# Kernel tuning notes

Hardware: AMD Instinct MI355X
Metric: run time of the kernel (lower is better)

## Reference

```python
import jax, jax.numpy as jnp
import numpy as np
from jax import lax

# Mamba2-130m-like config (quantized wrapper)
D_MODEL = 768
N_LAYER = 8
D_STATE = 128
D_CONV = 4
EXPAND = 2
HEADDIM = 64
VOCAB = 50288
D_INNER = EXPAND * D_MODEL            # 1536
NHEADS = D_INNER // HEADDIM           # 24
D_IN_PROJ = 2 * D_INNER + 2 * D_STATE + NHEADS  # 3352 (ngroups=1)
CONV_DIM = D_INNER + 2 * D_STATE      # 1792
EPS = 1e-5
BATCH, SEQLEN = 1, 1024

# QuantRMSNorm rsqrt lookup table (256 entries over [1e-5, 10])
LUT_X = jnp.linspace(1e-5, 10.0, 256)
LUT_Y = 1.0 / jnp.sqrt(LUT_X)


def _fake_quant_linear(w):
    # QuantLinear: torch.quantize_per_tensor(scale=0.1, zero_point=0, qint8).dequantize()
    return jnp.clip(jnp.round(w / 0.1), -128, 127) * 0.1


def setup_inputs():
    key = jax.random.key(0)
    ks = jax.random.split(key, 12)
    input_ids = jax.random.randint(ks[0], (BATCH, SEQLEN), 0, VOCAB)
    embedding = jax.random.normal(ks[1], (VOCAB, D_MODEL), jnp.float32)
    norm_w = jnp.ones((N_LAYER, D_MODEL), jnp.float32)
    in_proj_w = _fake_quant_linear(
        jax.random.normal(ks[2], (N_LAYER, D_IN_PROJ, D_MODEL), jnp.float32) * (D_MODEL ** -0.5))
    # QuantConv1d: asymmetric per-tensor int8 weight; forward uses q_weight.float()
    # WITHOUT subtracting zero_point (as in the source), times (w_scale * x_scale).
    conv_f = jax.random.normal(ks[3], (N_LAYER, CONV_DIM, D_CONV), jnp.float32) * (D_CONV ** -0.5)
    wmin = conv_f.min(axis=(1, 2), keepdims=True)
    wmax = conv_f.max(axis=(1, 2), keepdims=True)
    conv_scale = (wmax - wmin) / (255.0 + 1e-8)   # qmax - qmin = 255
    zp = jnp.round(-wmin / conv_scale)
    q_conv_w = jnp.clip(jnp.round(conv_f / conv_scale) + zp, -128, 127)
    conv_scale = conv_scale.reshape(N_LAYER)
    conv_b = jax.random.normal(ks[4], (N_LAYER, CONV_DIM), jnp.float32) * 0.02
    dt = jax.random.uniform(ks[5], (N_LAYER, NHEADS), jnp.float32, 0.001, 0.1)
    dt_bias = jnp.log(jnp.expm1(dt))              # inverse softplus
    A_log = jnp.log(jax.random.uniform(ks[6], (N_LAYER, NHEADS), jnp.float32, 1.0, 16.0))
    D_param = jnp.ones((N_LAYER, NHEADS), jnp.float32)
    mixer_norm_w = jnp.ones((N_LAYER, D_INNER), jnp.float32)
    out_proj_w = _fake_quant_linear(
        jax.random.normal(ks[7], (N_LAYER, D_MODEL, D_INNER), jnp.float32) * (D_INNER ** -0.5))
    normf_w = jnp.ones((D_MODEL,), jnp.float32)
    lm_head_w = _fake_quant_linear(
        jax.random.normal(ks[8], (VOCAB, D_MODEL), jnp.float32) * (D_MODEL ** -0.5))
    return dict(input_ids=input_ids, embedding=embedding, norm_w=norm_w, in_proj_w=in_proj_w,
                q_conv_w=q_conv_w, conv_scale=conv_scale, conv_b=conv_b, dt_bias=dt_bias,
                A_log=A_log, D_param=D_param, mixer_norm_w=mixer_norm_w, out_proj_w=out_proj_w,
                normf_w=normf_w, lm_head_w=lm_head_w)


def _lut_rmsnorm(x, w):
    # QuantRMSNorm: rsqrt approximated by a 256-entry LUT via bucketize
    rms = jnp.mean(x * x, axis=-1, keepdims=True) + EPS       # [b,l,1]
    idx = jnp.clip(jnp.searchsorted(LUT_X, rms), 0, 255)      # torch.bucketize (right=False)
    return x * LUT_Y[idx] * w


def _quant_act(x):
    # quantize_activation: symmetric per-tensor int8
    s = jnp.max(jnp.abs(x)) / (127.0 + 1e-8)
    return jnp.clip(jnp.round(x / s), -128, 127), s


def _mixer(u, in_w, qcw, cscale, cb, dtb, a_log, d_p, mnw, out_w):
    b, l, _ = u.shape
    zxbcdt = jnp.einsum('bld,ed->ble', u, in_w)               # QuantLinear (pre-fake-quantized w)
    z = zxbcdt[..., :D_INNER]
    xBC = zxbcdt[..., D_INNER:D_INNER + CONV_DIM]
    dt = jax.nn.softplus(zxbcdt[..., -NHEADS:] + dtb)         # [b,l,h]
    # QuantConv1d: depthwise causal conv on int8-quantized activation
    xq, xs = _quant_act(xBC)
    xp = jnp.pad(xq, ((0, 0), (D_CONV - 1, 0), (0, 0)))
    conv = sum(xp[:, k:k + l, :] * qcw[:, k] for k in range(D_CONV)) + cb
    xBC = jax.nn.silu(conv * (cscale * xs))
    x = xBC[..., :D_INNER].reshape(b, l, NHEADS, HEADDIM)
    Bm = xBC[..., D_INNER:D_INNER + D_STATE]                  # ngroups=1, shared over heads
    Cm = xBC[..., D_INNER + D_STATE:]
    dA = dt * (-jnp.exp(a_log))                               # [b,l,h]
    xdt = x * dt[..., None]
    def step(hs, inp):
        xdt_t, dA_t, B_t, C_t = inp
        hs = jnp.exp(dA_t)[..., None, None] * hs + xdt_t[..., None] * B_t[:, None, None, :]
        return hs, jnp.einsum('bhpn,bn->bhp', hs, C_t)
    h0 = jnp.zeros((b, NHEADS, HEADDIM, D_STATE), u.dtype)
    _, ys = lax.scan(step, h0, (xdt.swapaxes(0, 1), dA.swapaxes(0, 1),
                                Bm.swapaxes(0, 1), Cm.swapaxes(0, 1)))
    y = ys.swapaxes(0, 1) + x * d_p[None, None, :, None]      # [b,l,h,p]
    y = y.reshape(b, l, D_INNER)
    y = y * jax.nn.silu(z)                                    # gated RMSNorm (float, not LUT)
    y = y * lax.rsqrt(jnp.mean(y * y, axis=-1, keepdims=True) + EPS) * mnw
    return jnp.einsum('ble,de->bld', y, out_w)                # QuantLinear out_proj


def reference(input_ids, embedding, norm_w, in_proj_w, q_conv_w, conv_scale, conv_b,
              dt_bias, A_log, D_param, mixer_norm_w, out_proj_w, normf_w, lm_head_w):
    x = embedding[input_ids]
    for i in range(N_LAYER):
        y = _mixer(_lut_rmsnorm(x, norm_w[i]), in_proj_w[i], q_conv_w[i], conv_scale[i],
                   conv_b[i], dt_bias[i], A_log[i], D_param[i], mixer_norm_w[i], out_proj_w[i])
        x = y + x
    x = _lut_rmsnorm(x, normf_w)
    return jnp.einsum('bld,vd->blv', x, lm_head_w)            # logits [b,l,vocab]
```

## Files before the change

### kernel.cpp

```cpp
#include <hip/hip_runtime.h>
#include <math.h>

#define D_MODEL 768
#define N_LAYER 8
#define D_STATE 128
#define D_CONV 4
#define HEADDIM 64
#define D_INNER 1536
#define NHEADS 24
#define D_IN_PROJ 3352
#define CONV_DIM 1792
#define SEQLEN 1024
#define VOCAB 50288
#define EPS 1e-5f
#define T_SEG 32
#define NSEG  32
#define INP_PAD 3456
#define VOC_PAD 50304

typedef __bf16 bf16x8 __attribute__((ext_vector_type(8)));
typedef float f32x4 __attribute__((ext_vector_type(4)));

__device__ inline unsigned short f2bf(float x) {
    union { float f; unsigned u; } v; v.f = x;
    unsigned r = v.u + 0x7fffu + ((v.u >> 16) & 1u);
    return (unsigned short)(r >> 16);
}
__device__ inline float bf2f(unsigned short b) {
    union { unsigned u; float f; } v; v.u = ((unsigned)b) << 16;
    return v.f;
}

__device__ __forceinline__ void gld16(unsigned short* lds, const unsigned short* g) {
    __builtin_amdgcn_global_load_lds(
        (const __attribute__((address_space(1))) unsigned int*)g,
        (__attribute__((address_space(3))) unsigned int*)lds, 16, 0, 0);
}

__global__ void k_embed(const int* __restrict__ ids, const float* __restrict__ emb,
                        float* __restrict__ x) {
    int t = blockIdx.x;
    int id = ids[t];
    const float* er = emb + (long)id * D_MODEL;
    for (int d = threadIdx.x; d < D_MODEL; d += blockDim.x)
        x[(long)t * D_MODEL + d] = er[d];
}

__global__ void k_wq(const float* __restrict__ src, unsigned short* __restrict__ dst,
                     int n8_per_layer, int nlayer, long dst_stride8) {
    long total = (long)n8_per_layer * nlayer;
    for (long i = (long)blockIdx.x * 256 + threadIdx.x; i < total; i += (long)gridDim.x * 256) {
        long lay = i / n8_per_layer;
        long e = i - lay * n8_per_layer;
        const float* s = src + (lay * n8_per_layer + e) * 8;
        float4 a = *(const float4*)s, b = *(const float4*)(s + 4);
        float ff[8] = {a.x, a.y, a.z, a.w, b.x, b.y, b.z, b.w};
        unsigned short h[8];
#pragma unroll
        for (int j = 0; j < 8; ++j) h[j] = f2bf(rintf(ff[j] * 10.0f));
        *(uint4*)(dst + (lay * dst_stride8 + e) * 8) =
            make_uint4(h[0] | (h[1] << 16), h[2] | (h[3] << 16),
                       h[4] | (h[5] << 16), h[6] | (h[7] << 16));
    }
}

__global__ void k_lutnorm(const float* __restrict__ x, const float* __restrict__ w,
                          unsigned short* __restrict__ oh, unsigned short* __restrict__ ol,
                          unsigned* __restrict__ mx) {
    __shared__ float sbuf[256];
    int t = blockIdx.x;
    if (t == 0 && threadIdx.x == 0) *mx = 0u;
    const float* xr = x + (long)t * D_MODEL;
    float ss = 0.f;
    for (int d = threadIdx.x; d < D_MODEL; d += 256) { float v = xr[d]; ss += v * v; }
    sbuf[threadIdx.x] = ss; __syncthreads();
    for (int s = 128; s > 0; s >>= 1) {
        if (threadIdx.x < s) sbuf[threadIdx.x] += sbuf[threadIdx.x + s];
        __syncthreads();
    }
    float rms = sbuf[0] / (float)D_MODEL + EPS;
    const float X0 = 1e-5f;
    const float STEP = (10.0f - 1e-5f) / 255.0f;
    int idx = (int)ceilf((rms - X0) / STEP);
    idx = min(max(idx, 0), 255);
    while (idx > 0 && (X0 + (float)(idx - 1) * STEP) >= rms) --idx;
    while (idx < 255 && (X0 + (float)idx * STEP) < rms) ++idx;
    float scale = 1.0f / sqrtf(X0 + (float)idx * STEP);
    for (int d = threadIdx.x; d < D_MODEL; d += 256) {
        float v = xr[d] * scale * w[d];
        unsigned short h = f2bf(v);
        oh[(long)t * D_MODEL + d] = h;
        ol[(long)t * D_MODEL + d] = f2bf(v - bf2f(h));
    }
}

template <int BM, int BN, int PASSES, bool AMAX, bool ACCUM, int MT>
__global__ __launch_bounds__(256) void k_gemm(
    const unsigned short* __restrict__ Ah_g, const unsigned short* __restrict__ Al_g,
    const unsigned short* __restrict__ Bq_g, float* __restrict__ C,
    int N, int NT, int K, unsigned* __restrict__ mx) {

    const int i = blockIdx.x;
    const int rxcd = i & 7;
    const int xm = (i >> 3) % MT;
    const int q = i / (8 * MT);
    const int y = q * 8 + rxcd;
    if (y >= NT) return;
    const int bm = xm * BM, bn = y * BN;

    constexpr int MR = BM / 32;
    constexpr int NR = BN / 32;
    constexpr int ASL = 4 * BM;
    constexpr int BSL = 4 * BN;

    __shared__ __align__(16) unsigned short AhL[ASL * 8];
    __shared__ __align__(16) unsigned short AlL[(PASSES == 2) ? ASL * 8 : 8];
    __shared__ __align__(16) unsigned short BqL[BSL * 8];

    const int tid = threadIdx.x;
    const int w = tid >> 6, l = tid & 63;
    const int wm = w >> 1, wn = w & 1;
    const int lr = l & 15, lg = l >> 4;

    f32x4 acc[MR][NR];
#pragma unroll
    for (int m = 0; m < MR; ++m)
#pragma unroll
        for (int n = 0; n < NR; ++n) acc[m][n] = (f32x4){0.f, 0.f, 0.f, 0.f};

    for (int k0 = 0; k0 < K; k0 += 32) {
#pragma unroll
        for (int j = 0; j < ASL / 256; ++j) {
            int s = j * 256 + tid;
            int g = s / BM, r = s - g * BM;
            size_t goff = (size_t)(bm + r) * K + k0 + g * 8;
            gld16(&AhL[s * 8], Ah_g + goff);
            if constexpr (PASSES == 2) gld16(&AlL[s * 8], Al_g + goff);
        }
#pragma unroll
        for (int j = 0; j < BSL / 256; ++j) {
            int s = j * 256 + tid;
            int g = s / BN, r = s - g * BN;
            gld16(&BqL[s * 8], Bq_g + (size_t)(bn + r) * K + k0 + g * 8);
        }
        __syncthreads();

        bf16x8 ah[MR], al[MR], bh[NR];
#pragma unroll
        for (int m = 0; m < MR; ++m) {
            int row = wm * (BM / 2) + m * 16 + lr;
            ah[m] = *(const bf16x8*)&AhL[(lg * BM + row) * 8];
            if constexpr (PASSES == 2) al[m] = *(const bf16x8*)&AlL[(lg * BM + row) * 8];
        }
#pragma unroll
        for (int n = 0; n < NR; ++n) {
            int row = wn * (BN / 2) + n * 16 + lr;
            bh[n] = *(const bf16x8*)&BqL[(lg * BN + row) * 8];
        }
#pragma unroll
        for (int m = 0; m < MR; ++m)
#pragma unroll
            for (int n = 0; n < NR; ++n) {
                acc[m][n] = __builtin_amdgcn_mfma_f32_16x16x32_bf16(ah[m], bh[n], acc[m][n], 0, 0, 0);
                if constexpr (PASSES == 2)
                    acc[m][n] = __builtin_amdgcn_mfma_f32_16x16x32_bf16(al[m], bh[n], acc[m][n], 0, 0, 0);
            }
        __syncthreads();
    }

    float lmax = 0.f;
#pragma unroll
    for (int m = 0; m < MR; ++m) {
        int row0 = bm + wm * (BM / 2) + m * 16 + lg * 4;
#pragma unroll
        for (int n = 0; n < NR; ++n) {
            int col = bn + wn * (BN / 2) + n * 16 + lr;
            if (col < N) {
#pragma unroll
                for (int r4 = 0; r4 < 4; ++r4) {
                    float v = acc[m][n][r4] * 0.1f;
                    if (AMAX && col >= D_INNER) lmax = fmaxf(lmax, fabsf(v));
                    size_t off = (size_t)(row0 + r4) * N + col;
                    if (ACCUM) C[off] += v; else C[off] = v;
                }
            }
        }
    }
    if (AMAX) {
#pragma unroll
        for (int sh = 1; sh <= 32; sh <<= 1) lmax = fmaxf(lmax, __shfl_xor(lmax, sh));
        if (l == 0) atomicMax(mx, __float_as_uint(lmax));
    }
}

__global__ void k_convq(const float* __restrict__ zx, const float* __restrict__ qcw,
                        const float* __restrict__ cb, const float* __restrict__ cscale,
                        const unsigned* __restrict__ mx, float* __restrict__ xact) {
    int i = blockIdx.x * blockDim.x + threadIdx.x;
    if (i >= SEQLEN * CONV_DIM) return;
    float s = __uint_as_float(*mx) / (127.0f + 1e-8f);
    float inv_s = 1.0f / s;
    int t = i / CONV_DIM, c = i - t * CONV_DIM;
    float acc = cb[c];
#pragma unroll
    for (int k = 0; k < D_CONV; ++k) {
        int tt = t - (D_CONV - 1) + k;
        if (tt >= 0) {
            float q = rintf(zx[(size_t)tt * D_IN_PROJ + D_INNER + c] * inv_s);
            q = fminf(fmaxf(q, -128.0f), 127.0f);
            acc = fmaf(q, qcw[c * D_CONV + k], acc);
        }
    }
    float v = acc * (cscale[0] * s);
    xact[i] = v / (1.0f + expf(-v));
}

__global__ __launch_bounds__(256) void k_scan_local(
    const float* __restrict__ xact, const float* __restrict__ zx,
    const float* __restrict__ dtbias, const float* __restrict__ A_log,
    float* __restrict__ y, float* __restrict__ hloc, float* __restrict__ dpre) {
    const int head = blockIdx.x;
    const int seg  = blockIdx.y;
    const int tid  = threadIdx.x;
    const int p  = tid >> 2;
    const int nc = tid & 3;
    const int t0 = seg * T_SEG;

    __shared__ float4 sB4[T_SEG][32];
    __shared__ float4 sC4[T_SEG][32];
    __shared__ float  sX[T_SEG][64];
    __shared__ float  sDt[T_SEG], sA[T_SEG];

#pragma unroll
    for (int it = 0; it < 4; ++it) {
        int slot = tid + it * 256;
        int t = slot >> 5, c4 = slot & 31;
        const float* rowp = xact + (size_t)(t0 + t) * CONV_DIM + D_INNER;
        float4 bv = *(const float4*)(rowp + c4 * 4);
        float4 cv = *(const float4*)(rowp + D_STATE + c4 * 4);
        int grp = c4 >> 3, r4 = c4 & 7;
        int sl = grp * 8 + ((r4 + 2 * grp) & 7);
        sB4[t][sl] = bv;
        sC4[t][sl] = cv;
    }
#pragma unroll
    for (int it = 0; it < 2; ++it) {
        int slot = tid + it * 256;
        int t = slot >> 4, c4 = slot & 15;
        *(float4*)&sX[t][c4 * 4] =
            *(const float4*)(xact + (size_t)(t0 + t) * CONV_DIM + head * HEADDIM + c4 * 4);
    }
    if (tid < T_SEG) {
        float v = zx[(size_t)(t0 + tid) * D_IN_PROJ + (D_INNER + CONV_DIM) + head] + dtbias[head];
        float dtv = fmaxf(v, 0.f) + log1pf(expf(-fabsf(v)));
        sDt[tid] = dtv;
        sA[tid] = expf(dtv * (-expf(A_log[head])));
    }
    __syncthreads();

    float h[32];
#pragma unroll
    for (int j = 0; j < 32; ++j) h[j] = 0.f;
    float d = 1.f;
    float* yrow = y + head * HEADDIM + p;

    for (int t = 0; t < T_SEG; ++t) {
        float a = sA[t], dtv = sDt[t];
        float xdt = sX[t][p] * dtv;
        d *= a;
        float acc = 0.f;
#pragma unroll
        for (int j4 = 0; j4 < 8; ++j4) {
            int sl = nc * 8 + ((j4 + 2 * nc) & 7);
            float4 Bv = sB4[t][sl];
            float4 Cv = sC4[t][sl];
            h[j4 * 4 + 0] = fmaf(a, h[j4 * 4 + 0], xdt * Bv.x); acc = fmaf(h[j4 * 4 + 0], Cv.x, acc);
            h[j4 * 4 + 1] = fmaf(a, h[j4 * 4 + 1], xdt * Bv.y); acc = fmaf(h[j4 * 4 + 1], Cv.y, acc);
            h[j4 * 4 + 2] = fmaf(a, h[j4 * 4 + 2], xdt * Bv.z); acc = fmaf(h[j4 * 4 + 2], Cv.z, acc);
            h[j4 * 4 + 3] = fmaf(a, h[j4 * 4 + 3], xdt * Bv.w); acc = fmaf(h[j4 * 4 + 3], Cv.w, acc);
        }
        acc += __shfl_xor(acc, 1);
        acc += __shfl_xor(acc, 2);
        if (nc == 0) yrow[(size_t)(t0 + t) * D_INNER] = acc;
        if (tid == 0) dpre[(head * NSEG + seg) * T_SEG + t] = d;
    }

    float* hb = hloc + ((size_t)(head * NSEG + seg) * 64 + p) * 128 + nc * 32;
#pragma unroll
    for (int j4 = 0; j4 < 8; ++j4)
        *(float4*)(hb + j4 * 4) =
            make_float4(h[j4 * 4], h[j4 * 4 + 1], h[j4 * 4 + 2], h[j4 * 4 + 3]);
}

__global__ __launch_bounds__(256) void k_scan_seg(float* __restrict__ hloc,
                                                  const float* __restrict__ dpre) {
    int g = blockIdx.x * 256 + threadIdx.x;
    int head = g >> 11;
    int e4 = g & 2047;
    float4 run = make_float4(0.f, 0.f, 0.f, 0.f);
    for (int seg = 0; seg < NSEG; ++seg) {
        float d = dpre[(head * NSEG + seg) * T_SEG + (T_SEG - 1)];
        float4* ptr = (float4*)hloc + (size_t)(head * NSEG + seg) * 2048 + e4;
        float4 v = *ptr;
        run.x = fmaf(d, run.x, v.x);
        run.y = fmaf(d, run.y, v.y);
        run.z = fmaf(d, run.z, v.z);
        run.w = fmaf(d, run.w, v.w);
        *ptr = run;
    }
}

__global__ __launch_bounds__(256) void k_scan_fix(
    const float* __restrict__ xact, const float* __restrict__ hloc,
    const float* __restrict__ dpre, float* __restrict__ y) {
    const int head = blockIdx.x;
    const int seg  = blockIdx.y + 1;
    const int tid  = threadIdx.x;
    const int p  = tid >> 2;
    const int nc = tid & 3;
    const int t0 = seg * T_SEG;

    __shared__ float4 sC4[T_SEG][32];
    __shared__ float  sD[T_SEG];

#pragma unroll
    for (int it = 0; it < 4; ++it) {
        int slot = tid + it * 256;
        int t = slot >> 5, c4 = slot & 31;
        float4 cv = *(const float4*)(xact + (size_t)(t0 + t) * CONV_DIM + D_INNER + D_STATE + c4 * 4);
        int grp = c4 >> 3, r4 = c4 & 7;
        sC4[t][grp * 8 + ((r4 + 2 * grp) & 7)] = cv;
    }
    if (tid < T_SEG) sD[tid] = dpre[(head * NSEG + seg) * T_SEG + tid];
    __syncthreads();

    float H[32];
    const float* hb = hloc + ((size_t)(head * NSEG + seg - 1) * 64 + p) * 128 + nc * 32;
#pragma unroll
    for (int j4 = 0; j4 < 8; ++j4) {
        float4 v = *(const float4*)(hb + j4 * 4);
        H[j4 * 4 + 0] = v.x; H[j4 * 4 + 1] = v.y; H[j4 * 4 + 2] = v.z; H[j4 * 4 + 3] = v.w;
    }
    float* yrow = y + head * HEADDIM + p;
    for (int t = 0; t < T_SEG; ++t) {
        float acc = 0.f;
#pragma unroll
        for (int j4 = 0; j4 < 8; ++j4) {
            int sl = nc * 8 + ((j4 + 2 * nc) & 7);
            float4 Cv = sC4[t][sl];
            acc = fmaf(H[j4 * 4 + 0], Cv.x, acc);
            acc = fmaf(H[j4 * 4 + 1], Cv.y, acc);
            acc = fmaf(H[j4 * 4 + 2], Cv.z, acc);
            acc = fmaf(H[j4 * 4 + 3], Cv.w, acc);
        }
        acc += __shfl_xor(acc, 1);
        acc += __shfl_xor(acc, 2);
        if (nc == 0) yrow[(size_t)(t0 + t) * D_INNER] += sD[t] * acc;
    }
}

__global__ void k_gatenorm(const float* __restrict__ ybuf, const float* __restrict__ zx,
                           const float* __restrict__ xact, const float* __restrict__ dpar,
                           const float* __restrict__ mnw,
                           unsigned short* __restrict__ y3h, unsigned short* __restrict__ y3l) {
    __shared__ float sbuf[256];
    int t = blockIdx.x;
    const float* yr = ybuf + (long)t * D_INNER;
    const float* zr = zx + (long)t * D_IN_PROJ;
    const float* xa = xact + (long)t * CONV_DIM;
    float vals[6];
    float ss = 0.f;
#pragma unroll
    for (int j = 0; j < 6; ++j) {
        int e = threadIdx.x + j * 256;
        float z = zr[e];
        float v = (yr[e] + xa[e] * dpar[e >> 6]) * (z / (1.0f + expf(-z)));
        vals[j] = v; ss += v * v;
    }
    sbuf[threadIdx.x] = ss; __syncthreads();
    for (int s = 128; s > 0; s >>= 1) {
        if (threadIdx.x < s) sbuf[threadIdx.x] += sbuf[threadIdx.x + s];
        __syncthreads();
    }
    float scale = 1.0f / sqrtf(sbuf[0] / (float)D_INNER + EPS);
#pragma unroll
    for (int j = 0; j < 6; ++j) {
        int e = threadIdx.x + j * 256;
        float v = vals[j] * scale * mnw[e];
        unsigned short h = f2bf(v);
        y3h[(long)t * D_INNER + e] = h;
        y3l[(long)t * D_INNER + e] = f2bf(v - bf2f(h));
    }
}

extern "C" void kernel_launch(void* const* d_in, const int* in_sizes, int n_in,
                              void* d_out, int out_size, void* d_ws, size_t ws_size,
                              hipStream_t stream) {
    const int*   ids    = (const int*)d_in[0];
    const float* emb    = (const float*)d_in[1];
    const float* norm_w = (const float*)d_in[2];
    const float* inw    = (const float*)d_in[3];
    const float* qconv  = (const float*)d_in[4];
    const float* cscale = (const float*)d_in[5];
    const float* convb  = (const float*)d_in[6];
    const float* dtbias = (const float*)d_in[7];
    const float* alog   = (const float*)d_in[8];
    const float* dpar   = (const float*)d_in[9];
    const float* mnw    = (const float*)d_in[10];
    const float* outw   = (const float*)d_in[11];
    const float* normf  = (const float*)d_in[12];
    const float* lmw    = (const float*)d_in[13];
    float* out = (float*)d_out;

    char* base = (char*)d_ws;
    size_t off = 0;
    auto alloc = [&](size_t bytes) { char* r = base + off; off = (off + bytes + 255) & ~(size_t)255; return r; };

    float* xres = (float*)alloc((size_t)SEQLEN * D_MODEL * 4);
    float* zx   = (float*)alloc((size_t)SEQLEN * D_IN_PROJ * 4);
    float* xact = (float*)alloc((size_t)SEQLEN * CONV_DIM * 4);
    float* ybuf = (float*)alloc((size_t)SEQLEN * D_INNER * 4);
    float* hloc = (float*)alloc((size_t)NHEADS * NSEG * HEADDIM * D_STATE * 4);
    float* dpre = (float*)alloc((size_t)NHEADS * NSEG * T_SEG * 4);
    unsigned* mx = (unsigned*)alloc(64);
    unsigned short* uh  = (unsigned short*)alloc((size_t)SEQLEN * D_MODEL * 2);
    unsigned short* ul  = (unsigned short*)alloc((size_t)SEQLEN * D_MODEL * 2);
    unsigned short* y3h = (unsigned short*)alloc((size_t)SEQLEN * D_INNER * 2);
    unsigned short* y3l = (unsigned short*)alloc((size_t)SEQLEN * D_INNER * 2);
    unsigned short* inwq  = (unsigned short*)alloc((size_t)N_LAYER * INP_PAD * D_MODEL * 2);
    unsigned short* outwq = (unsigned short*)alloc((size_t)N_LAYER * D_MODEL * D_INNER * 2);
    unsigned short* lmwq  = (unsigned short*)alloc((size_t)VOC_PAD * D_MODEL * 2);

    k_embed<<<SEQLEN, 256, 0, stream>>>(ids, emb, xres);
    k_wq<<<2048, 256, 0, stream>>>(inw, inwq, D_IN_PROJ * D_MODEL / 8, N_LAYER,
                                   (long)INP_PAD * D_MODEL / 8);
    k_wq<<<2048, 256, 0, stream>>>(outw, outwq, D_MODEL * D_INNER / 8, N_LAYER,
                                   (long)D_MODEL * D_INNER / 8);
    k_wq<<<2048, 256, 0, stream>>>(lmw, lmwq, VOCAB * D_MODEL / 8, 1,
                                   (long)VOC_PAD * D_MODEL / 8);

    int nq = SEQLEN * CONV_DIM;
    for (int l = 0; l < N_LAYER; ++l) {
        k_lutnorm<<<SEQLEN, 256, 0, stream>>>(xres, norm_w + l * D_MODEL, uh, ul, mx);
        k_gemm<128, 128, 2, true, false, 8><<<256, 256, 0, stream>>>(
            uh, ul, inwq + (size_t)l * INP_PAD * D_MODEL, zx, D_IN_PROJ, 27, D_MODEL, mx);
        k_convq<<<(nq + 255) / 256, 256, 0, stream>>>(zx, qconv + l * CONV_DIM * D_CONV,
                                                      convb + l * CONV_DIM, cscale + l, mx, xact);
        dim3 gs1(NHEADS, NSEG);
        k_scan_local<<<gs1, 256, 0, stream>>>(xact, zx, dtbias + l * NHEADS, alog + l * NHEADS,
                                              ybuf, hloc, dpre);
        k_scan_seg<<<192, 256, 0, stream>>>(hloc, dpre);
        dim3 gs3(NHEADS, NSEG - 1);
        k_scan_fix<<<gs3, 256, 0, stream>>>(xact, hloc, dpre, ybuf);
        k_gatenorm<<<SEQLEN, 256, 0, stream>>>(ybuf, zx, xact, dpar + l * NHEADS,
                                               mnw + l * D_INNER, y3h, y3l);
        k_gemm<64, 64, 2, false, true, 16><<<256, 256, 0, stream>>>(
            y3h, y3l, outwq + (size_t)l * D_MODEL * D_INNER, xres, D_MODEL, 12, D_INNER, nullptr);
    }
    k_lutnorm<<<SEQLEN, 256, 0, stream>>>(xres, normf, uh, ul, mx);
    k_gemm<128, 128, 1, false, false, 8><<<3200, 256, 0, stream>>>(
        uh, nullptr, lmwq, out, VOCAB, 393, D_MODEL, nullptr);
}
```

Measured before the change: 1.738 ms.

## Replace LDS-staged GEMM with register-direct MFMA GEMM and split-K atomics

Rewrites the GEMM so each wave loads its A and B fragments straight from global memory into registers and prefetches the next k-step, dropping LDS staging and block-wide barriers. Out_proj switches to split-K with atomicAdd into the residual, and the in_proj and lm_head tiles are resized, with weight padding enlarged to match. Without LDS, operands are no longer shared across waves, so global and L2 traffic goes up. Atomics make the accumulation order nondeterministic. NK is hardcoded to 24, which only matches K/KSPLIT=768.

```diff
diff --git a/kernel.cpp b/kernel.cpp
--- a/kernel.cpp
+++ b/kernel.cpp
@@ -15,8 +15,8 @@
 #define EPS 1e-5f
 #define T_SEG 32
 #define NSEG  32
-#define INP_PAD 3456
-#define VOC_PAD 50304
+#define INP_PAD2 3584
+#define VOC_PAD2 50432
 
 typedef __bf16 bf16x8 __attribute__((ext_vector_type(8)));
 typedef float f32x4 __attribute__((ext_vector_type(4)));
@@ -30,11 +30,8 @@
     union { unsigned u; float f; } v; v.u = ((unsigned)b) << 16;
     return v.f;
 }
-
-__device__ __forceinline__ void gld16(unsigned short* lds, const unsigned short* g) {
-    __builtin_amdgcn_global_load_lds(
-        (const __attribute__((address_space(1))) unsigned int*)g,
-        (__attribute__((address_space(3))) unsigned int*)lds, 16, 0, 0);
+__device__ __forceinline__ bf16x8 asbf8(uint4 v) {
+    return __builtin_bit_cast(bf16x8, v);
 }
 
 __global__ void k_embed(const int* __restrict__ ids, const float* __restrict__ emb,
@@ -94,94 +91,106 @@
     }
 }
 
-template <int BM, int BN, int PASSES, bool AMAX, bool ACCUM, int MT>
-__global__ __launch_bounds__(256) void k_gemm(
+template <int WMR, int WNR, int PASSES, bool AMAX, int KSPLIT, bool ATOMIC, int MTILES>
+__global__ __launch_bounds__(256) void k_gemm_reg(
     const unsigned short* __restrict__ Ah_g, const unsigned short* __restrict__ Al_g,
     const unsigned short* __restrict__ Bq_g, float* __restrict__ C,
-    int N, int NT, int K, unsigned* __restrict__ mx) {
+    int N, int NCT, int K, unsigned* __restrict__ mx) {
 
     const int i = blockIdx.x;
     const int rxcd = i & 7;
-    const int xm = (i >> 3) % MT;
-    const int q = i / (8 * MT);
-    const int y = q * 8 + rxcd;
-    if (y >= NT) return;
-    const int bm = xm * BM, bn = y * BN;
-
-    constexpr int MR = BM / 32;
-    constexpr int NR = BN / 32;
-    constexpr int ASL = 4 * BM;
-    constexpr int BSL = 4 * BN;
-
-    __shared__ __align__(16) unsigned short AhL[ASL * 8];
-    __shared__ __align__(16) unsigned short AlL[(PASSES == 2) ? ASL * 8 : 8];
-    __shared__ __align__(16) unsigned short BqL[BSL * 8];
+    int rest = i >> 3;
+    const int xm = rest % MTILES; rest /= MTILES;
+    const int ks = rest % KSPLIT; rest /= KSPLIT;
+    const int y = rest * 8 + rxcd;
+    if (y >= NCT) return;
 
     const int tid = threadIdx.x;
     const int w = tid >> 6, l = tid & 63;
-    const int wm = w >> 1, wn = w & 1;
     const int lr = l & 15, lg = l >> 4;
 
-    f32x4 acc[MR][NR];
-#pragma unroll
-    for (int m = 0; m < MR; ++m)
-#pragma unroll
-        for (int n = 0; n < NR; ++n) acc[m][n] = (f32x4){0.f, 0.f, 0.f, 0.f};
-
-    for (int k0 = 0; k0 < K; k0 += 32) {
-#pragma unroll
-        for (int j = 0; j < ASL / 256; ++j) {
-            int s = j * 256 + tid;
-            int g = s / BM, r = s - g * BM;
-            size_t goff = (size_t)(bm + r) * K + k0 + g * 8;
-            gld16(&AhL[s * 8], Ah_g + goff);
-            if constexpr (PASSES == 2) gld16(&AlL[s * 8], Al_g + goff);
-        }
-#pragma unroll
-        for (int j = 0; j < BSL / 256; ++j) {
-            int s = j * 256 + tid;
-            int g = s / BN, r = s - g * BN;
-            gld16(&BqL[s * 8], Bq_g + (size_t)(bn + r) * K + k0 + g * 8);
-        }
-        __syncthreads();
-
-        bf16x8 ah[MR], al[MR], bh[NR];
-#pragma unroll
-        for (int m = 0; m < MR; ++m) {
-            int row = wm * (BM / 2) + m * 16 + lr;
-            ah[m] = *(const bf16x8*)&AhL[(lg * BM + row) * 8];
-            if constexpr (PASSES == 2) al[m] = *(const bf16x8*)&AlL[(lg * BM + row) * 8];
-        }
-#pragma unroll
-        for (int n = 0; n < NR; ++n) {
-            int row = wn * (BN / 2) + n * 16 + lr;
-            bh[n] = *(const bf16x8*)&BqL[(lg * BN + row) * 8];
-        }
-#pragma unroll
-        for (int m = 0; m < MR; ++m)
-#pragma unroll
-            for (int n = 0; n < NR; ++n) {
-                acc[m][n] = __builtin_amdgcn_mfma_f32_16x16x32_bf16(ah[m], bh[n], acc[m][n], 0, 0, 0);
+    const int bm = xm * (WMR * 16);
+    const int bn = y * (4 * WNR * 16) + w * (WNR * 16);
+    const int kbeg = ks * (K / KSPLIT);
+    constexpr int NK = 24;
+
+    const unsigned short* ah_p[WMR];
+    const unsigned short* al_p[WMR];
+    const unsigned short* b_p[WNR];
+#pragma unroll
+    for (int m = 0; m < WMR; ++m) {
+        size_t off = (size_t)(bm + m * 16 + lr) * K + kbeg + lg * 8;
+        ah_p[m] = Ah_g + off;
+        if constexpr (PASSES == 2) al_p[m] = Al_g + off;
+    }
+#pragma unroll
+    for (int n = 0; n < WNR; ++n)
+        b_p[n] = Bq_g + (size_t)(bn + n * 16 + lr) * K + kbeg + lg * 8;
+
+    f32x4 acc[WMR][WNR];
+#pragma unroll
+    for (int m = 0; m < WMR; ++m)
+#pragma unroll
+        for (int n = 0; n < WNR; ++n) acc[m][n] = (f32x4){0.f, 0.f, 0.f, 0.f};
+
+    uint4 ca[PASSES][WMR], cb[WNR];
+#pragma unroll
+    for (int m = 0; m < WMR; ++m) {
+        ca[0][m] = *(const uint4*)(ah_p[m]);
+        if constexpr (PASSES == 2) ca[1][m] = *(const uint4*)(al_p[m]);
+    }
+#pragma unroll
+    for (int n = 0; n < WNR; ++n) cb[n] = *(const uint4*)(b_p[n]);
+
+#pragma unroll
+    for (int kt = 0; kt < NK; ++kt) {
+        uint4 na[PASSES][WMR], nb[WNR];
+        if (kt + 1 < NK) {
+            const int ko = (kt + 1) * 32;
+#pragma unroll
+            for (int m = 0; m < WMR; ++m) {
+                na[0][m] = *(const uint4*)(ah_p[m] + ko);
+                if constexpr (PASSES == 2) na[1][m] = *(const uint4*)(al_p[m] + ko);
+            }
+#pragma unroll
+            for (int n = 0; n < WNR; ++n) nb[n] = *(const uint4*)(b_p[n] + ko);
+        }
+#pragma unroll
+        for (int m = 0; m < WMR; ++m)
+#pragma unroll
+            for (int n = 0; n < WNR; ++n) {
+                acc[m][n] = __builtin_amdgcn_mfma_f32_16x16x32_bf16(
+                    asbf8(ca[0][m]), asbf8(cb[n]), acc[m][n], 0, 0, 0);
                 if constexpr (PASSES == 2)
-                    acc[m][n] = __builtin_amdgcn_mfma_f32_16x16x32_bf16(al[m], bh[n], acc[m][n], 0, 0, 0);
+                    acc[m][n] = __builtin_amdgcn_mfma_f32_16x16x32_bf16(
+                        asbf8(ca[1][m]), asbf8(cb[n]), acc[m][n], 0, 0, 0);
             }
-        __syncthreads();
+        if (kt + 1 < NK) {
+#pragma unroll
+            for (int m = 0; m < WMR; ++m) {
+                ca[0][m] = na[0][m];
+                if constexpr (PASSES == 2) ca[1][m] = na[1][m];
+            }
+#pragma unroll
+            for (int n = 0; n < WNR; ++n) cb[n] = nb[n];
+        }
     }
 
     float lmax = 0.f;
 #pragma unroll
-    for (int m = 0; m < MR; ++m) {
-        int row0 = bm + wm * (BM / 2) + m * 16 + lg * 4;
-#pragma unroll
-        for (int n = 0; n < NR; ++n) {
-            int col = bn + wn * (BN / 2) + n * 16 + lr;
+    for (int m = 0; m < WMR; ++m) {
+        int row0 = bm + m * 16 + lg * 4;
+#pragma unroll
+        for (int n = 0; n < WNR; ++n) {
+            int col = bn + n * 16 + lr;
             if (col < N) {
 #pragma unroll
                 for (int r4 = 0; r4 < 4; ++r4) {
                     float v = acc[m][n][r4] * 0.1f;
-                    if (AMAX && col >= D_INNER) lmax = fmaxf(lmax, fabsf(v));
+                    if (AMAX && col >= D_INNER && col < D_INNER + CONV_DIM)
+                        lmax = fmaxf(lmax, fabsf(v));
                     size_t off = (size_t)(row0 + r4) * N + col;
-                    if (ACCUM) C[off] += v; else C[off] = v;
+                    if (ATOMIC) atomicAdd(&C[off], v); else C[off] = v;
                 }
             }
         }
@@ -427,23 +436,23 @@
     unsigned short* ul  = (unsigned short*)alloc((size_t)SEQLEN * D_MODEL * 2);
     unsigned short* y3h = (unsigned short*)alloc((size_t)SEQLEN * D_INNER * 2);
     unsigned short* y3l = (unsigned short*)alloc((size_t)SEQLEN * D_INNER * 2);
-    unsigned short* inwq  = (unsigned short*)alloc((size_t)N_LAYER * INP_PAD * D_MODEL * 2);
+    unsigned short* inwq  = (unsigned short*)alloc((size_t)N_LAYER * INP_PAD2 * D_MODEL * 2);
     unsigned short* outwq = (unsigned short*)alloc((size_t)N_LAYER * D_MODEL * D_INNER * 2);
-    unsigned short* lmwq  = (unsigned short*)alloc((size_t)VOC_PAD * D_MODEL * 2);
+    unsigned short* lmwq  = (unsigned short*)alloc((size_t)VOC_PAD2 * D_MODEL * 2);
 
     k_embed<<<SEQLEN, 256, 0, stream>>>(ids, emb, xres);
     k_wq<<<2048, 256, 0, stream>>>(inw, inwq, D_IN_PROJ * D_MODEL / 8, N_LAYER,
-                                   (long)INP_PAD * D_MODEL / 8);
+                                   (long)INP_PAD2 * D_MODEL / 8);
     k_wq<<<2048, 256, 0, stream>>>(outw, outwq, D_MODEL * D_INNER / 8, N_LAYER,
                                    (long)D_MODEL * D_INNER / 8);
     k_wq<<<2048, 256, 0, stream>>>(lmw, lmwq, VOCAB * D_MODEL / 8, 1,
-                                   (long)VOC_PAD * D_MODEL / 8);
+                                   (long)VOC_PAD2 * D_MODEL / 8);
 
     int nq = SEQLEN * CONV_DIM;
     for (int l = 0; l < N_LAYER; ++l) {
         k_lutnorm<<<SEQLEN, 256, 0, stream>>>(xres, norm_w + l * D_MODEL, uh, ul, mx);
-        k_gemm<128, 128, 2, true, false, 8><<<256, 256, 0, stream>>>(
-            uh, ul, inwq + (size_t)l * INP_PAD * D_MODEL, zx, D_IN_PROJ, 27, D_MODEL, mx);
+        k_gemm_reg<4, 2, 2, true, 1, false, 16><<<512, 256, 0, stream>>>(
+            uh, ul, inwq + (size_t)l * INP_PAD2 * D_MODEL, zx, D_IN_PROJ, 28, D_MODEL, mx);
         k_convq<<<(nq + 255) / 256, 256, 0, stream>>>(zx, qconv + l * CONV_DIM * D_CONV,
                                                       convb + l * CONV_DIM, cscale + l, mx, xact);
         dim3 gs1(NHEADS, NSEG);
@@ -454,10 +463,10 @@
         k_scan_fix<<<gs3, 256, 0, stream>>>(xact, hloc, dpre, ybuf);
         k_gatenorm<<<SEQLEN, 256, 0, stream>>>(ybuf, zx, xact, dpar + l * NHEADS,
                                                mnw + l * D_INNER, y3h, y3l);
-        k_gemm<64, 64, 2, false, true, 16><<<256, 256, 0, stream>>>(
-            y3h, y3l, outwq + (size_t)l * D_MODEL * D_INNER, xres, D_MODEL, 12, D_INNER, nullptr);
+        k_gemm_reg<2, 2, 2, false, 2, true, 32><<<512, 256, 0, stream>>>(
+            y3h, y3l, outwq + (size_t)l * D_MODEL * D_INNER, xres, D_MODEL, 6, D_INNER, nullptr);
     }
     k_lutnorm<<<SEQLEN, 256, 0, stream>>>(xres, normf, uh, ul, mx);
-    k_gemm<128, 128, 1, false, false, 8><<<3200, 256, 0, stream>>>(
-        uh, nullptr, lmwq, out, VOCAB, 393, D_MODEL, nullptr);
-}
+    k_gemm_reg<4, 4, 1, false, 1, false, 16><<<3200, 256, 0, stream>>>(
+        uh, nullptr, lmwq, out, VOCAB, 197, D_MODEL, nullptr);
+}
```

After: 1.967 ms. 1.13x slower.
